# Kernel tuning notes

Hardware: AMD Instinct MI355X
Metric: run time of the kernel (lower is better)

## Reference

```python
import jax, jax.numpy as jnp
import numpy as np

N_HIGH = 4096
N_LOW = 262144
E_HIGH = 65536
E_LOW = 524288
IN_DIM = 128
OUT_DIM = 128
HEADS = 4
HEAD_DIM = OUT_DIM // HEADS
EPS = 1e-5
SCALE = np.float32(1.0 / np.sqrt(HEAD_DIM))


def _layernorm(x, w, b):
    m = jnp.mean(x, axis=-1, keepdims=True)
    v = jnp.var(x, axis=-1, keepdims=True)
    return (x - m) * jax.lax.rsqrt(v + EPS) * w + b


def _transformer_conv(x, edge_index, Wq, bq, Wk, bk, Wv, bv, Wskip, bskip, num_nodes):
    # PyG TransformerConv: q from target node, k/v from source node, per-head
    # softmax over incoming edges, concat heads, plus skip connection.
    q = (x @ Wq + bq).reshape(num_nodes, HEADS, HEAD_DIM)
    k = (x @ Wk + bk).reshape(num_nodes, HEADS, HEAD_DIM)
    v = (x @ Wv + bv).reshape(num_nodes, HEADS, HEAD_DIM)
    src, dst = edge_index[0], edge_index[1]
    score = jnp.einsum('ehd,ehd->eh', q[dst], k[src]) * SCALE  # [E, H]
    m = jax.ops.segment_max(score, dst, num_segments=num_nodes)
    e = jnp.exp(score - m[dst])
    denom = jax.ops.segment_sum(e, dst, num_segments=num_nodes)
    alpha = e / denom[dst]
    agg = jax.ops.segment_sum(alpha[:, :, None] * v[src], dst, num_segments=num_nodes)
    return agg.reshape(num_nodes, OUT_DIM) + x @ Wskip + bskip


def setup_inputs() -> dict:
    key = jax.random.key(0)
    ks = jax.random.split(key, 12)
    sw = np.float32(1.0 / np.sqrt(IN_DIM))
    sa = np.float32(1.0 / np.sqrt(2 * OUT_DIM))
    return {
        'high_emb': jax.random.normal(ks[0], (N_HIGH, IN_DIM), jnp.float32),
        'low_emb': jax.random.normal(ks[1], (N_LOW, IN_DIM), jnp.float32),
        'Wq': jax.random.normal(ks[2], (IN_DIM, OUT_DIM), jnp.float32) * sw,
        'bq': jnp.zeros((OUT_DIM,), jnp.float32),
        'Wk': jax.random.normal(ks[3], (IN_DIM, OUT_DIM), jnp.float32) * sw,
        'bk': jnp.zeros((OUT_DIM,), jnp.float32),
        'Wv': jax.random.normal(ks[4], (IN_DIM, OUT_DIM), jnp.float32) * sw,
        'bv': jnp.zeros((OUT_DIM,), jnp.float32),
        'Wskip': jax.random.normal(ks[5], (IN_DIM, OUT_DIM), jnp.float32) * sw,
        'bskip': jnp.zeros((OUT_DIM,), jnp.float32),
        'ln_w': jnp.ones((OUT_DIM,), jnp.float32),
        'ln_b': jnp.zeros((OUT_DIM,), jnp.float32),
        'w_lh': jax.random.normal(ks[6], (2 * OUT_DIM, 1), jnp.float32) * sa,
        'w_hl': jax.random.normal(ks[7], (2 * OUT_DIM, 1), jnp.float32) * sa,
        'edge_index_high': jax.random.randint(ks[8], (2, E_HIGH), 0, N_HIGH, jnp.int32),
        'edge_index_low': jax.random.randint(ks[9], (2, E_LOW), 0, N_LOW, jnp.int32),
        'batch': jnp.sort(jax.random.randint(ks[10], (N_LOW,), 0, N_HIGH, jnp.int32)),
    }


def reference(high_emb, low_emb, Wq, bq, Wk, bk, Wv, bv, Wskip, bskip, ln_w, ln_b, w_lh, w_hl, edge_index_high, edge_index_low, batch):
    h = _transformer_conv(high_emb, edge_index_high, Wq, bq, Wk, bk, Wv, bv, Wskip, bskip, N_HIGH)
    l = _transformer_conv(low_emb, edge_index_low, Wq, bq, Wk, bk, Wv, bv, Wskip, bskip, N_LOW)
    h = jax.nn.relu(_layernorm(h, ln_w, ln_b))
    l = jax.nn.relu(_layernorm(l, ln_w, ln_b))
    # global_mean_pool over low nodes per graph
    counts = jax.ops.segment_sum(jnp.ones((N_LOW,), jnp.float32), batch, num_segments=N_HIGH)
    pooled = jax.ops.segment_sum(l, batch, num_segments=N_HIGH) / jnp.maximum(counts, 1.0)[:, None]
    sim = jax.nn.sigmoid(jnp.concatenate([h, pooled], axis=1) @ w_lh)  # [N_HIGH, 1]
    high_out = sim * h + (1.0 - sim) * pooled
    # vectorized form of the per-graph loop: broadcast high node to its low nodes
    hb = h[batch]  # [N_LOW, OUT_DIM]
    a = jax.nn.sigmoid(jnp.concatenate([hb, l], axis=1) @ w_hl)  # [N_LOW, 1]
    low_out = a * l + (1.0 - a) * hb
    return (high_out, low_out)
```

## Files before the change

kernel.cpp:

```cpp
#include <hip/hip_runtime.h>
#include <hip/hip_bf16.h>
#include <math.h>

#define N_HIGH 4096
#define N_LOW 262144
#define E_HIGH 65536
#define E_LOW 524288
#define LN_EPS 1e-5f
#define ATT_SCALE 0.17677669529663687f

typedef short bf16x8 __attribute__((ext_vector_type(8)));
typedef float f32x4 __attribute__((ext_vector_type(4)));

__device__ __forceinline__ float bf2f(unsigned int u) {
    union { unsigned int i; float f; } v; v.i = u << 16; return v.f;
}
__device__ __forceinline__ unsigned short f2bf(float f) {
    union { unsigned int i; float f; } v; v.f = f;
    unsigned int r = (v.i + 0x7fffu + ((v.i >> 16) & 1u)) >> 16;
    return (unsigned short)r;
}
__device__ __forceinline__ float ldf(const void* p, size_t i, int isbf) {
    if (isbf) return bf2f(((const unsigned short*)p)[i]);
    return ((const float*)p)[i];
}
__device__ __forceinline__ float4 load4f(const void* p, size_t i, int isbf) {
    if (isbf) {
        uint2 u = *(const uint2*)((const unsigned short*)p + i);
        float4 r;
        r.x = bf2f(u.x & 0xffffu); r.y = bf2f(u.x >> 16);
        r.z = bf2f(u.y & 0xffffu); r.w = bf2f(u.y >> 16);
        return r;
    }
    return *(const float4*)((const float*)p + i);
}
__device__ __forceinline__ void stf(void* p, size_t i, float v, int isbf) {
    if (isbf) ((unsigned short*)p)[i] = f2bf(v);
    else      ((float*)p)[i] = v;
}

__global__ __launch_bounds__(256) void probe_dtype_kernel(
    const unsigned int* __restrict__ x, int* __restrict__ flag)
{
    __shared__ int cnt;
    if (threadIdx.x == 0) cnt = 0;
    __syncthreads();
    unsigned int b = (x[threadIdx.x] >> 8) & 0x7fu;
    if (b >= 60u && b <= 65u) atomicAdd(&cnt, 1);
    __syncthreads();
    if (threadIdx.x == 0) *flag = (cnt >= 128) ? 1 : 0;
}

__global__ __launch_bounds__(256) void prep_wt_kernel(
    const void* __restrict__ Wq, const void* __restrict__ Wk,
    const void* __restrict__ Wv, const void* __restrict__ Ws,
    unsigned short* __restrict__ Wt, const int* __restrict__ dflag)
{
    const int isbf = *dflag;
    const int g = blockIdx.x >> 3;
    const int slice = blockIdx.x & 7;
    const void* W = (g == 0) ? Wq : (g == 1) ? Wk : (g == 2) ? Wv : Ws;
    #pragma unroll
    for (int i = 0; i < 8; ++i) {
        int linear = i * 256 + threadIdx.x;
        int k = slice * 16 + (linear >> 7);
        int n = linear & 127;
        float v = ldf(W, (size_t)k * 128 + n, isbf);
        Wt[((size_t)g * 128 + n) * 128 + k] = f2bf(v);
    }
}

__global__ __launch_bounds__(256) void gemm_mfma_kernel(
    const void* __restrict__ x, const unsigned short* __restrict__ Wt,
    const void* __restrict__ bq, const void* __restrict__ bk,
    const void* __restrict__ bv, const void* __restrict__ bs,
    unsigned short* __restrict__ qkv, float* __restrict__ accv,
    const int* __restrict__ dflag)
{
    __shared__ unsigned short As[64 * 136];
    __shared__ unsigned short Bs[128 * 136];
    const int isbf = *dflag;
    const int tid = threadIdx.x;
    const int m0 = blockIdx.x * 64;

    #pragma unroll
    for (int i = 0; i < 8; ++i) {
        int linear = i * 256 + tid;
        int row = linear >> 5;
        int c4 = (linear & 31) << 2;
        float4 v = load4f(x, (size_t)(m0 + row) * 128 + c4, isbf);
        ushort4 s;
        s.x = f2bf(v.x); s.y = f2bf(v.y); s.z = f2bf(v.z); s.w = f2bf(v.w);
        *(ushort4*)&As[row * 136 + c4] = s;
    }

    const void* blist[4] = { bq, bk, bv, bs };

    const int lane = tid & 63;
    const int w = tid >> 6;
    const int wm = (w & 1) * 32;
    const int wn = (w >> 1) * 64;
    const int lr = lane & 15;
    const int lk = (lane >> 4) * 8;
    const int rbase = (lane >> 4) * 4;

    for (int c = 0; c < 4; ++c) {
        __syncthreads();
        #pragma unroll
        for (int i = 0; i < 8; ++i) {
            int linear = i * 256 + tid;
            int n = linear >> 4;
            int c8 = (linear & 15) << 3;
            uint4 v = *(const uint4*)&Wt[((size_t)c * 128 + n) * 128 + c8];
            *(uint4*)&Bs[n * 136 + c8] = v;
        }
        __syncthreads();

        f32x4 acc[2][4];
        #pragma unroll
        for (int a = 0; a < 2; ++a)
            #pragma unroll
            for (int b = 0; b < 4; ++b) acc[a][b] = (f32x4){0.f, 0.f, 0.f, 0.f};

        #pragma unroll
        for (int kk = 0; kk < 4; ++kk) {
            int k0 = kk * 32 + lk;
            bf16x8 af[2], bfv[4];
            #pragma unroll
            for (int im = 0; im < 2; ++im)
                af[im] = *(const bf16x8*)&As[(wm + im * 16 + lr) * 136 + k0];
            #pragma unroll
            for (int in = 0; in < 4; ++in)
                bfv[in] = *(const bf16x8*)&Bs[(wn + in * 16 + lr) * 136 + k0];
            #pragma unroll
            for (int im = 0; im < 2; ++im)
                #pragma unroll
                for (int in = 0; in < 4; ++in)
                    acc[im][in] = __builtin_amdgcn_mfma_f32_16x16x32_bf16(
                        af[im], bfv[in], acc[im][in], 0, 0, 0);
        }

        float bias[4];
        #pragma unroll
        for (int in = 0; in < 4; ++in) bias[in] = ldf(blist[c], wn + in * 16 + lr, isbf);

        #pragma unroll
        for (int im = 0; im < 2; ++im) {
            #pragma unroll
            for (int r = 0; r < 4; ++r) {
                int m = wm + im * 16 + rbase + r;
                size_t row = (size_t)(m0 + m);
                #pragma unroll
                for (int in = 0; in < 4; ++in) {
                    int n = wn + in * 16 + lr;
                    float val = acc[im][in][r] + bias[in];
                    if (c < 3) qkv[row * 384 + c * 128 + n] = f2bf(val);
                    else       accv[row * 128 + n] = val;
                }
            }
        }
    }
}

__global__ __launch_bounds__(256) void count_deg_kernel(
    const int* __restrict__ ei, int E, int* __restrict__ deg)
{
    int e = blockIdx.x * 256 + threadIdx.x;
    if (e >= E) return;
    atomicAdd(&deg[ei[E + e]], 1);
}

__global__ __launch_bounds__(256) void scan1_kernel(
    const int* __restrict__ deg, int* __restrict__ pre, int* __restrict__ bsum)
{
    __shared__ int wsum[4];
    int tid = threadIdx.x;
    int lane = tid & 63, w = tid >> 6;
    int base = blockIdx.x * 1024 + tid * 4;
    int4 v = *(const int4*)(deg + base);
    int s = v.x + v.y + v.z + v.w;
    int inc = s;
    #pragma unroll
    for (int m = 1; m < 64; m <<= 1) {
        int t = __shfl_up(inc, m, 64);
        if (lane >= m) inc += t;
    }
    if (lane == 63) wsum[w] = inc;
    __syncthreads();
    int woff = 0;
    #pragma unroll
    for (int j = 0; j < 4; ++j) if (j < w) woff += wsum[j];
    int excl = woff + inc - s;
    pre[base]     = excl;
    pre[base + 1] = excl + v.x;
    pre[base + 2] = excl + v.x + v.y;
    pre[base + 3] = excl + v.x + v.y + v.z;
    if (tid == 0) bsum[blockIdx.x] = wsum[0] + wsum[1] + wsum[2] + wsum[3];
}

__global__ void scan2_kernel(int* __restrict__ bsum, int NB)
{
    if (threadIdx.x == 0 && blockIdx.x == 0) {
        int run = 0;
        for (int i = 0; i < NB; ++i) { int t = bsum[i]; bsum[i] = run; run += t; }
    }
}

__global__ __launch_bounds__(256) void scan3_kernel(
    const int* __restrict__ pre, const int* __restrict__ bsum,
    int* __restrict__ off, int N)
{
    int i = blockIdx.x * 256 + threadIdx.x;
    if (i >= N) return;
    off[i] = pre[i] + bsum[i >> 10];
}

__global__ __launch_bounds__(256) void fill_csr_kernel(
    const int* __restrict__ ei, int E, int* __restrict__ off,
    int* __restrict__ csr)
{
    int e = blockIdx.x * 256 + threadIdx.x;
    if (e >= E) return;
    int dst = ei[E + e];
    int pos = atomicAdd(&off[dst], 1);
    csr[pos] = ei[e];
}

__global__ __launch_bounds__(256) void attn_gather_ln_kernel(
    const unsigned short* __restrict__ qkv, const int* __restrict__ csr_src,
    const int* __restrict__ off_end, const int* __restrict__ deg,
    const float* skip, const void* __restrict__ lnw,
    const void* __restrict__ lnb, unsigned short* out, int N,
    const int* __restrict__ dflag)
{
    const int isbf = *dflag;
    int lane = threadIdx.x & 63;
    int n = blockIdx.x * 4 + (threadIdx.x >> 6);
    if (n >= N) return;
    int end = off_end[n];
    int cnt = deg[n];
    int p = end - cnt;

    ushort2 qv = *(const ushort2*)(qkv + (long)n * 384 + 2 * lane);
    float q0 = bf2f(qv.x), q1 = bf2f(qv.y);
    float den = 0.f, a0 = 0.f, a1 = 0.f;

    for (; p + 1 < end; p += 2) {
        int s0 = csr_src[p], s1 = csr_src[p + 1];
        const unsigned short* b0 = qkv + (long)s0 * 384 + 2 * lane;
        const unsigned short* b1 = qkv + (long)s1 * 384 + 2 * lane;
        ushort2 k0 = *(const ushort2*)(b0 + 128);
        ushort2 k1 = *(const ushort2*)(b1 + 128);
        ushort2 v0 = *(const ushort2*)(b0 + 256);
        ushort2 v1 = *(const ushort2*)(b1 + 256);
        float p0 = q0 * bf2f(k0.x) + q1 * bf2f(k0.y);
        float p1 = q0 * bf2f(k1.x) + q1 * bf2f(k1.y);
        #pragma unroll
        for (int m = 1; m < 16; m <<= 1) {
            p0 += __shfl_xor(p0, m, 64);
            p1 += __shfl_xor(p1, m, 64);
        }
        float z0 = fminf(fmaxf(p0 * ATT_SCALE, -60.f), 60.f);
        float z1 = fminf(fmaxf(p1 * ATT_SCALE, -60.f), 60.f);
        float e0 = __expf(z0), e1 = __expf(z1);
        den += e0 + e1;
        a0 += e0 * bf2f(v0.x) + e1 * bf2f(v1.x);
        a1 += e0 * bf2f(v0.y) + e1 * bf2f(v1.y);
    }
    if (p < end) {
        int s0 = csr_src[p];
        const unsigned short* b0 = qkv + (long)s0 * 384 + 2 * lane;
        ushort2 k0 = *(const ushort2*)(b0 + 128);
        ushort2 v0 = *(const ushort2*)(b0 + 256);
        float p0 = q0 * bf2f(k0.x) + q1 * bf2f(k0.y);
        #pragma unroll
        for (int m = 1; m < 16; m <<= 1) p0 += __shfl_xor(p0, m, 64);
        float z0 = fminf(fmaxf(p0 * ATT_SCALE, -60.f), 60.f);
        float e0 = __expf(z0);
        den += e0;
        a0 += e0 * bf2f(v0.x);
        a1 += e0 * bf2f(v0.y);
    }

    float inv = (cnt > 0) ? 1.f / den : 0.f;
    float2 sk = *(const float2*)(skip + (long)n * 128 + 2 * lane);
    float x0 = a0 * inv + sk.x;
    float x1 = a1 * inv + sk.y;

    float s = x0 + x1, qq = x0 * x0 + x1 * x1;
    #pragma unroll
    for (int m = 1; m < 64; m <<= 1) {
        s += __shfl_xor(s, m, 64);
        qq += __shfl_xor(qq, m, 64);
    }
    float mean = s * (1.f / 128.f);
    float var = fmaxf(qq * (1.f / 128.f) - mean * mean, 0.f);
    float rs = rsqrtf(var + LN_EPS);
    float w0 = ldf(lnw, 2 * lane, isbf), w1 = ldf(lnw, 2 * lane + 1, isbf);
    float bb0 = ldf(lnb, 2 * lane, isbf), bb1 = ldf(lnb, 2 * lane + 1, isbf);
    float y0 = fmaxf((x0 - mean) * rs * w0 + bb0, 0.f);
    float y1 = fmaxf((x1 - mean) * rs * w1 + bb1, 0.f);
    unsigned short* o = out + (long)n * 256 + 2 * lane;
    o[0] = f2bf(y0);
    o[1] = f2bf(y1);
}

__global__ __launch_bounds__(128) void pool_kernel(
    const unsigned short* __restrict__ l, const int* __restrict__ batch,
    float* __restrict__ pooled)
{
    __shared__ int se[2];
    int g = blockIdx.x;
    if (threadIdx.x == 0) {
        int lo = 0, hi = N_LOW;
        while (lo < hi) { int mid = (lo + hi) >> 1; if (batch[mid] < g) lo = mid + 1; else hi = mid; }
        se[0] = lo;
        hi = N_LOW;
        while (lo < hi) { int mid = (lo + hi) >> 1; if (batch[mid] < g + 1) lo = mid + 1; else hi = mid; }
        se[1] = lo;
    }
    __syncthreads();
    int start = se[0], end = se[1];
    int d = threadIdx.x;
    float ssum = 0.f;
    for (int r = start; r < end; ++r) ssum += bf2f(l[(long)r * 256 + d]);
    int cnt = end - start;
    pooled[(long)g * 128 + d] = ssum / (float)(cnt > 0 ? cnt : 1);
}

__global__ __launch_bounds__(256) void high_out_kernel(
    const unsigned short* __restrict__ h, const float* __restrict__ pooled,
    const void* __restrict__ wlh, void* __restrict__ out,
    const int* __restrict__ dflag)
{
    const int isbf = *dflag;
    int lane = threadIdx.x & 63;
    int n = blockIdx.x * 4 + (threadIdx.x >> 6);
    if (n >= N_HIGH) return;
    float h0 = bf2f(h[(long)n * 256 + 2 * lane]);
    float h1 = bf2f(h[(long)n * 256 + 2 * lane + 1]);
    float2 pv = *(const float2*)(pooled + (long)n * 128 + 2 * lane);
    float s = h0 * ldf(wlh, 2 * lane, isbf) + h1 * ldf(wlh, 2 * lane + 1, isbf)
            + pv.x * ldf(wlh, 128 + 2 * lane, isbf) + pv.y * ldf(wlh, 128 + 2 * lane + 1, isbf);
    #pragma unroll
    for (int m = 1; m < 64; m <<= 1) s += __shfl_xor(s, m, 64);
    float sim = 1.f / (1.f + __expf(-s));
    stf(out, (size_t)n * 128 + 2 * lane,     sim * h0 + (1.f - sim) * pv.x, isbf);
    stf(out, (size_t)n * 128 + 2 * lane + 1, sim * h1 + (1.f - sim) * pv.y, isbf);
}

__global__ __launch_bounds__(256) void low_out_kernel(
    const unsigned short* __restrict__ l, const unsigned short* __restrict__ h,
    const int* __restrict__ batch, const void* __restrict__ whl,
    void* __restrict__ out, const int* __restrict__ dflag)
{
    const int isbf = *dflag;
    int lane = threadIdx.x & 63;
    int n = blockIdx.x * 4 + (threadIdx.x >> 6);
    if (n >= N_LOW) return;
    int g = batch[n];
    float l0 = bf2f(l[(long)n * 256 + 2 * lane]);
    float l1 = bf2f(l[(long)n * 256 + 2 * lane + 1]);
    float h0 = bf2f(h[(long)g * 256 + 2 * lane]);
    float h1 = bf2f(h[(long)g * 256 + 2 * lane + 1]);
    float s = h0 * ldf(whl, 2 * lane, isbf) + h1 * ldf(whl, 2 * lane + 1, isbf)
            + l0 * ldf(whl, 128 + 2 * lane, isbf) + l1 * ldf(whl, 128 + 2 * lane + 1, isbf);
    #pragma unroll
    for (int m = 1; m < 64; m <<= 1) s += __shfl_xor(s, m, 64);
    float a = 1.f / (1.f + __expf(-s));
    size_t base = (size_t)N_HIGH * 128 + (size_t)n * 128 + 2 * lane;
    stf(out, base,     a * l0 + (1.f - a) * h0, isbf);
    stf(out, base + 1, a * l1 + (1.f - a) * h1, isbf);
}

extern "C" void kernel_launch(void* const* d_in, const int* in_sizes, int n_in,
                              void* d_out, int out_size, void* d_ws, size_t ws_size,
                              hipStream_t stream)
{
    const void* high_emb = d_in[0];
    const void* low_emb  = d_in[1];
    const void* Wq = d_in[2];  const void* bq = d_in[3];
    const void* Wk = d_in[4];  const void* bk = d_in[5];
    const void* Wv = d_in[6];  const void* bv = d_in[7];
    const void* Ws = d_in[8];  const void* bs = d_in[9];
    const void* ln_w = d_in[10];
    const void* ln_b = d_in[11];
    const void* w_lh = d_in[12];
    const void* w_hl = d_in[13];
    const int* ei_high = (const int*)d_in[14];
    const int* ei_low  = (const int*)d_in[15];
    const int* batch   = (const int*)d_in[16];

    char* ws = (char*)d_ws;
    const size_t OFF_QKV_LOW  = 0;
    const size_t OFF_ACC_LOW  = 201326592;
    const size_t OFF_AUX      = 335544320;
    const size_t OFF_QKV_HIGH = 348127232;
    const size_t OFF_ACC_HIGH = 351272960;
    const size_t OFF_POOLED   = 354484224;
    const size_t OFF_FLAG     = 356581376;
    const size_t WS_NEEDED    = 356581632;
    if (ws_size < WS_NEEDED) return;

    unsigned short* qkv_low  = (unsigned short*)(ws + OFF_QKV_LOW);
    float*          acc_low  = (float*)(ws + OFF_ACC_LOW);
    unsigned short* qkv_high = (unsigned short*)(ws + OFF_QKV_HIGH);
    float*          acc_high = (float*)(ws + OFF_ACC_HIGH);
    float*          pooled   = (float*)(ws + OFF_POOLED);
    int*            dflag    = (int*)(ws + OFF_FLAG);

    unsigned short* Wt       = (unsigned short*)(ws + OFF_AUX);
    int* deg_low  = (int*)(ws + OFF_AUX +  262144);
    int* pre_low  = (int*)(ws + OFF_AUX + 1310720);
    int* off_low  = (int*)(ws + OFF_AUX + 2359296);
    int* csr_low  = (int*)(ws + OFF_AUX + 3407872);
    int* deg_high = (int*)(ws + OFF_AUX + 5505024);
    int* pre_high = (int*)(ws + OFF_AUX + 5521408);
    int* off_high = (int*)(ws + OFF_AUX + 5537792);
    int* csr_high = (int*)(ws + OFF_AUX + 5554176);
    int* bsum     = (int*)(ws + OFF_AUX + 5816320);

    unsigned short* l_low  = (unsigned short*)acc_low;
    unsigned short* h_high = (unsigned short*)acc_high;

    hipMemsetAsync(deg_low, 0, (size_t)N_LOW * sizeof(int), stream);
    hipMemsetAsync(deg_high, 0, (size_t)N_HIGH * sizeof(int), stream);

    probe_dtype_kernel<<<1, 256, 0, stream>>>((const unsigned int*)high_emb, dflag);

    count_deg_kernel<<<E_LOW / 256, 256, 0, stream>>>(ei_low, E_LOW, deg_low);
    count_deg_kernel<<<E_HIGH / 256, 256, 0, stream>>>(ei_high, E_HIGH, deg_high);

    scan1_kernel<<<N_LOW / 1024, 256, 0, stream>>>(deg_low, pre_low, bsum);
    scan2_kernel<<<1, 64, 0, stream>>>(bsum, N_LOW / 1024);
    scan3_kernel<<<N_LOW / 256, 256, 0, stream>>>(pre_low, bsum, off_low, N_LOW);

    scan1_kernel<<<N_HIGH / 1024, 256, 0, stream>>>(deg_high, pre_high, bsum);
    scan2_kernel<<<1, 64, 0, stream>>>(bsum, N_HIGH / 1024);
    scan3_kernel<<<N_HIGH / 256, 256, 0, stream>>>(pre_high, bsum, off_high, N_HIGH);

    fill_csr_kernel<<<E_LOW / 256, 256, 0, stream>>>(ei_low, E_LOW, off_low, csr_low);
    fill_csr_kernel<<<E_HIGH / 256, 256, 0, stream>>>(ei_high, E_HIGH, off_high, csr_high);

    prep_wt_kernel<<<32, 256, 0, stream>>>(Wq, Wk, Wv, Ws, Wt, dflag);

    gemm_mfma_kernel<<<N_HIGH / 64, 256, 0, stream>>>(
        high_emb, Wt, bq, bk, bv, bs, qkv_high, acc_high, dflag);
    gemm_mfma_kernel<<<N_LOW / 64, 256, 0, stream>>>(
        low_emb, Wt, bq, bk, bv, bs, qkv_low, acc_low, dflag);

    attn_gather_ln_kernel<<<N_HIGH / 4, 256, 0, stream>>>(
        qkv_high, csr_high, off_high, deg_high, acc_high, ln_w, ln_b,
        h_high, N_HIGH, dflag);
    attn_gather_ln_kernel<<<N_LOW / 4, 256, 0, stream>>>(
        qkv_low, csr_low, off_low, deg_low, acc_low, ln_w, ln_b,
        l_low, N_LOW, dflag);

    pool_kernel<<<N_HIGH, 128, 0, stream>>>(l_low, batch, pooled);

    high_out_kernel<<<N_HIGH / 4, 256, 0, stream>>>(h_high, pooled, w_lh, d_out, dflag);
    low_out_kernel<<<N_LOW / 4, 256, 0, stream>>>(l_low, h_high, batch, w_hl, d_out, dflag);
}
```

Baseline: 763.3 us.

## Store skip in bf16, use 16 lanes per node with 16-byte vector gathers

The skip-connection output of the GEMM is now written as bf16 instead of fp32, and the layer-norm result overwrites it in place with a 128-element row stride. The attention-gather, layernorm and low-output kernels move from one 64-lane wave per node to 16 lanes per node, each lane loading 8 bf16 values with uint4 loads. LayerNorm weights and w_hl are pre-converted to fp32 once by an extra block in prep_wt. The aim is fewer gather transactions, fewer shuffle reduction steps and less skip/output traffic. The cost is extra bf16 rounding of the skip term.

```diff
diff --git a/kernel.cpp b/kernel.cpp
--- a/kernel.cpp
+++ b/kernel.cpp
@@ -38,6 +38,20 @@
     if (isbf) ((unsigned short*)p)[i] = f2bf(v);
     else      ((float*)p)[i] = v;
 }
+__device__ __forceinline__ void unpack8(uint4 u, float* f) {
+    f[0] = bf2f(u.x & 0xffffu); f[1] = bf2f(u.x >> 16);
+    f[2] = bf2f(u.y & 0xffffu); f[3] = bf2f(u.y >> 16);
+    f[4] = bf2f(u.z & 0xffffu); f[5] = bf2f(u.z >> 16);
+    f[6] = bf2f(u.w & 0xffffu); f[7] = bf2f(u.w >> 16);
+}
+__device__ __forceinline__ uint4 pack8(const float* f) {
+    uint4 u;
+    u.x = (unsigned)f2bf(f[0]) | ((unsigned)f2bf(f[1]) << 16);
+    u.y = (unsigned)f2bf(f[2]) | ((unsigned)f2bf(f[3]) << 16);
+    u.z = (unsigned)f2bf(f[4]) | ((unsigned)f2bf(f[5]) << 16);
+    u.w = (unsigned)f2bf(f[6]) | ((unsigned)f2bf(f[7]) << 16);
+    return u;
+}
 
 __global__ __launch_bounds__(256) void probe_dtype_kernel(
     const unsigned int* __restrict__ x, int* __restrict__ flag)
@@ -54,9 +68,18 @@
 __global__ __launch_bounds__(256) void prep_wt_kernel(
     const void* __restrict__ Wq, const void* __restrict__ Wk,
     const void* __restrict__ Wv, const void* __restrict__ Ws,
-    unsigned short* __restrict__ Wt, const int* __restrict__ dflag)
+    const void* __restrict__ lnw, const void* __restrict__ lnb,
+    const void* __restrict__ whl,
+    unsigned short* __restrict__ Wt, float* __restrict__ lnwbf,
+    float* __restrict__ whlf, const int* __restrict__ dflag)
 {
     const int isbf = *dflag;
+    if (blockIdx.x >= 32) {
+        int t = threadIdx.x;
+        lnwbf[t] = (t < 128) ? ldf(lnw, t, isbf) : ldf(lnb, t - 128, isbf);
+        whlf[t] = ldf(whl, t, isbf);
+        return;
+    }
     const int g = blockIdx.x >> 3;
     const int slice = blockIdx.x & 7;
     const void* W = (g == 0) ? Wq : (g == 1) ? Wk : (g == 2) ? Wv : Ws;
@@ -74,7 +97,7 @@
     const void* __restrict__ x, const unsigned short* __restrict__ Wt,
     const void* __restrict__ bq, const void* __restrict__ bk,
     const void* __restrict__ bv, const void* __restrict__ bs,
-    unsigned short* __restrict__ qkv, float* __restrict__ accv,
+    unsigned short* __restrict__ qkv, unsigned short* __restrict__ accv,
     const int* __restrict__ dflag)
 {
     __shared__ unsigned short As[64 * 136];
@@ -155,7 +178,7 @@
                     int n = wn + in * 16 + lr;
                     float val = acc[im][in][r] + bias[in];
                     if (c < 3) qkv[row * 384 + c * 128 + n] = f2bf(val);
-                    else       accv[row * 128 + n] = val;
+                    else       accv[row * 128 + n] = f2bf(val);
                 }
             }
         }
@@ -229,80 +252,91 @@
 __global__ __launch_bounds__(256) void attn_gather_ln_kernel(
     const unsigned short* __restrict__ qkv, const int* __restrict__ csr_src,
     const int* __restrict__ off_end, const int* __restrict__ deg,
-    const float* skip, const void* __restrict__ lnw,
-    const void* __restrict__ lnb, unsigned short* out, int N,
-    const int* __restrict__ dflag)
-{
-    const int isbf = *dflag;
-    int lane = threadIdx.x & 63;
-    int n = blockIdx.x * 4 + (threadIdx.x >> 6);
+    unsigned short* skip_out, const float* __restrict__ lnwbf, int N)
+{
+    int il = threadIdx.x & 15;
+    int n = blockIdx.x * 16 + (threadIdx.x >> 4);
     if (n >= N) return;
     int end = off_end[n];
     int cnt = deg[n];
     int p = end - cnt;
 
-    ushort2 qv = *(const ushort2*)(qkv + (long)n * 384 + 2 * lane);
-    float q0 = bf2f(qv.x), q1 = bf2f(qv.y);
-    float den = 0.f, a0 = 0.f, a1 = 0.f;
-
-    for (; p + 1 < end; p += 2) {
-        int s0 = csr_src[p], s1 = csr_src[p + 1];
-        const unsigned short* b0 = qkv + (long)s0 * 384 + 2 * lane;
-        const unsigned short* b1 = qkv + (long)s1 * 384 + 2 * lane;
-        ushort2 k0 = *(const ushort2*)(b0 + 128);
-        ushort2 k1 = *(const ushort2*)(b1 + 128);
-        ushort2 v0 = *(const ushort2*)(b0 + 256);
-        ushort2 v1 = *(const ushort2*)(b1 + 256);
-        float p0 = q0 * bf2f(k0.x) + q1 * bf2f(k0.y);
-        float p1 = q0 * bf2f(k1.x) + q1 * bf2f(k1.y);
-        #pragma unroll
-        for (int m = 1; m < 16; m <<= 1) {
-            p0 += __shfl_xor(p0, m, 64);
-            p1 += __shfl_xor(p1, m, 64);
-        }
-        float z0 = fminf(fmaxf(p0 * ATT_SCALE, -60.f), 60.f);
-        float z1 = fminf(fmaxf(p1 * ATT_SCALE, -60.f), 60.f);
-        float e0 = __expf(z0), e1 = __expf(z1);
+    float qf[8];
+    unpack8(*(const uint4*)(qkv + (long)n * 384 + 8 * il), qf);
+    float acc[8] = {0.f, 0.f, 0.f, 0.f, 0.f, 0.f, 0.f, 0.f};
+    float den = 0.f;
+
+    int it = 0;
+    for (; it + 1 < cnt; it += 2) {
+        int s0 = csr_src[p + it];
+        int s1 = csr_src[p + it + 1];
+        const unsigned short* b0 = qkv + (long)s0 * 384 + 8 * il;
+        const unsigned short* b1 = qkv + (long)s1 * 384 + 8 * il;
+        uint4 k0w = *(const uint4*)(b0 + 128);
+        uint4 v0w = *(const uint4*)(b0 + 256);
+        uint4 k1w = *(const uint4*)(b1 + 128);
+        uint4 v1w = *(const uint4*)(b1 + 256);
+        float kf[8], vf[8], kg[8], vg[8];
+        unpack8(k0w, kf); unpack8(v0w, vf);
+        unpack8(k1w, kg); unpack8(v1w, vg);
+        float p0 = 0.f, p1 = 0.f;
+        #pragma unroll
+        for (int j = 0; j < 8; ++j) { p0 += qf[j] * kf[j]; p1 += qf[j] * kg[j]; }
+        p0 += __shfl_xor(p0, 1, 64); p1 += __shfl_xor(p1, 1, 64);
+        p0 += __shfl_xor(p0, 2, 64); p1 += __shfl_xor(p1, 2, 64);
+        float e0 = __expf(fminf(fmaxf(p0 * ATT_SCALE, -60.f), 60.f));
+        float e1 = __expf(fminf(fmaxf(p1 * ATT_SCALE, -60.f), 60.f));
         den += e0 + e1;
-        a0 += e0 * bf2f(v0.x) + e1 * bf2f(v1.x);
-        a1 += e0 * bf2f(v0.y) + e1 * bf2f(v1.y);
-    }
-    if (p < end) {
-        int s0 = csr_src[p];
-        const unsigned short* b0 = qkv + (long)s0 * 384 + 2 * lane;
-        ushort2 k0 = *(const ushort2*)(b0 + 128);
-        ushort2 v0 = *(const ushort2*)(b0 + 256);
-        float p0 = q0 * bf2f(k0.x) + q1 * bf2f(k0.y);
-        #pragma unroll
-        for (int m = 1; m < 16; m <<= 1) p0 += __shfl_xor(p0, m, 64);
-        float z0 = fminf(fmaxf(p0 * ATT_SCALE, -60.f), 60.f);
-        float e0 = __expf(z0);
+        #pragma unroll
+        for (int j = 0; j < 8; ++j) acc[j] += e0 * vf[j] + e1 * vg[j];
+    }
+    if (it < cnt) {
+        int s0 = csr_src[p + it];
+        const unsigned short* b0 = qkv + (long)s0 * 384 + 8 * il;
+        uint4 k0w = *(const uint4*)(b0 + 128);
+        uint4 v0w = *(const uint4*)(b0 + 256);
+        float kf[8], vf[8];
+        unpack8(k0w, kf); unpack8(v0w, vf);
+        float p0 = 0.f;
+        #pragma unroll
+        for (int j = 0; j < 8; ++j) p0 += qf[j] * kf[j];
+        p0 += __shfl_xor(p0, 1, 64);
+        p0 += __shfl_xor(p0, 2, 64);
+        float e0 = __expf(fminf(fmaxf(p0 * ATT_SCALE, -60.f), 60.f));
         den += e0;
-        a0 += e0 * bf2f(v0.x);
-        a1 += e0 * bf2f(v0.y);
+        #pragma unroll
+        for (int j = 0; j < 8; ++j) acc[j] += e0 * vf[j];
     }
 
     float inv = (cnt > 0) ? 1.f / den : 0.f;
-    float2 sk = *(const float2*)(skip + (long)n * 128 + 2 * lane);
-    float x0 = a0 * inv + sk.x;
-    float x1 = a1 * inv + sk.y;
-
-    float s = x0 + x1, qq = x0 * x0 + x1 * x1;
-    #pragma unroll
-    for (int m = 1; m < 64; m <<= 1) {
+    float x[8];
+    unpack8(*(const uint4*)(skip_out + (long)n * 128 + 8 * il), x);
+    float s = 0.f, qq = 0.f;
+    #pragma unroll
+    for (int j = 0; j < 8; ++j) {
+        x[j] = acc[j] * inv + x[j];
+        s += x[j];
+        qq += x[j] * x[j];
+    }
+    #pragma unroll
+    for (int m = 1; m < 16; m <<= 1) {
         s += __shfl_xor(s, m, 64);
         qq += __shfl_xor(qq, m, 64);
     }
     float mean = s * (1.f / 128.f);
     float var = fmaxf(qq * (1.f / 128.f) - mean * mean, 0.f);
     float rs = rsqrtf(var + LN_EPS);
-    float w0 = ldf(lnw, 2 * lane, isbf), w1 = ldf(lnw, 2 * lane + 1, isbf);
-    float bb0 = ldf(lnb, 2 * lane, isbf), bb1 = ldf(lnb, 2 * lane + 1, isbf);
-    float y0 = fmaxf((x0 - mean) * rs * w0 + bb0, 0.f);
-    float y1 = fmaxf((x1 - mean) * rs * w1 + bb1, 0.f);
-    unsigned short* o = out + (long)n * 256 + 2 * lane;
-    o[0] = f2bf(y0);
-    o[1] = f2bf(y1);
+    float4 wA = *(const float4*)(lnwbf + 8 * il);
+    float4 wB = *(const float4*)(lnwbf + 8 * il + 4);
+    float4 bA = *(const float4*)(lnwbf + 128 + 8 * il);
+    float4 bB = *(const float4*)(lnwbf + 128 + 8 * il + 4);
+    float wv[8] = {wA.x, wA.y, wA.z, wA.w, wB.x, wB.y, wB.z, wB.w};
+    float bv[8] = {bA.x, bA.y, bA.z, bA.w, bB.x, bB.y, bB.z, bB.w};
+    float y[8];
+    #pragma unroll
+    for (int j = 0; j < 8; ++j)
+        y[j] = fmaxf((x[j] - mean) * rs * wv[j] + bv[j], 0.f);
+    *(uint4*)(skip_out + (long)n * 128 + 8 * il) = pack8(y);
 }
 
 __global__ __launch_bounds__(128) void pool_kernel(
@@ -322,10 +356,17 @@
     __syncthreads();
     int start = se[0], end = se[1];
     int d = threadIdx.x;
-    float ssum = 0.f;
-    for (int r = start; r < end; ++r) ssum += bf2f(l[(long)r * 256 + d]);
+    float s0 = 0.f, s1 = 0.f, s2 = 0.f, s3 = 0.f;
+    int r = start;
+    for (; r + 3 < end; r += 4) {
+        s0 += bf2f(l[(long)r * 128 + d]);
+        s1 += bf2f(l[(long)(r + 1) * 128 + d]);
+        s2 += bf2f(l[(long)(r + 2) * 128 + d]);
+        s3 += bf2f(l[(long)(r + 3) * 128 + d]);
+    }
+    for (; r < end; ++r) s0 += bf2f(l[(long)r * 128 + d]);
     int cnt = end - start;
-    pooled[(long)g * 128 + d] = ssum / (float)(cnt > 0 ? cnt : 1);
+    pooled[(long)g * 128 + d] = ((s0 + s1) + (s2 + s3)) / (float)(cnt > 0 ? cnt : 1);
 }
 
 __global__ __launch_bounds__(256) void high_out_kernel(
@@ -337,8 +378,8 @@
     int lane = threadIdx.x & 63;
     int n = blockIdx.x * 4 + (threadIdx.x >> 6);
     if (n >= N_HIGH) return;
-    float h0 = bf2f(h[(long)n * 256 + 2 * lane]);
-    float h1 = bf2f(h[(long)n * 256 + 2 * lane + 1]);
+    float h0 = bf2f(h[(long)n * 128 + 2 * lane]);
+    float h1 = bf2f(h[(long)n * 128 + 2 * lane + 1]);
     float2 pv = *(const float2*)(pooled + (long)n * 128 + 2 * lane);
     float s = h0 * ldf(wlh, 2 * lane, isbf) + h1 * ldf(wlh, 2 * lane + 1, isbf)
             + pv.x * ldf(wlh, 128 + 2 * lane, isbf) + pv.y * ldf(wlh, 128 + 2 * lane + 1, isbf);
@@ -351,26 +392,39 @@
 
 __global__ __launch_bounds__(256) void low_out_kernel(
     const unsigned short* __restrict__ l, const unsigned short* __restrict__ h,
-    const int* __restrict__ batch, const void* __restrict__ whl,
+    const int* __restrict__ batch, const float* __restrict__ whlf,
     void* __restrict__ out, const int* __restrict__ dflag)
 {
     const int isbf = *dflag;
-    int lane = threadIdx.x & 63;
-    int n = blockIdx.x * 4 + (threadIdx.x >> 6);
+    int il = threadIdx.x & 15;
+    int n = blockIdx.x * 16 + (threadIdx.x >> 4);
     if (n >= N_LOW) return;
     int g = batch[n];
-    float l0 = bf2f(l[(long)n * 256 + 2 * lane]);
-    float l1 = bf2f(l[(long)n * 256 + 2 * lane + 1]);
-    float h0 = bf2f(h[(long)g * 256 + 2 * lane]);
-    float h1 = bf2f(h[(long)g * 256 + 2 * lane + 1]);
-    float s = h0 * ldf(whl, 2 * lane, isbf) + h1 * ldf(whl, 2 * lane + 1, isbf)
-            + l0 * ldf(whl, 128 + 2 * lane, isbf) + l1 * ldf(whl, 128 + 2 * lane + 1, isbf);
-    #pragma unroll
-    for (int m = 1; m < 64; m <<= 1) s += __shfl_xor(s, m, 64);
+    float lf[8], hf[8];
+    unpack8(*(const uint4*)(l + (long)n * 128 + 8 * il), lf);
+    unpack8(*(const uint4*)(h + (long)g * 128 + 8 * il), hf);
+    float4 wh0 = *(const float4*)(whlf + 8 * il);
+    float4 wh1 = *(const float4*)(whlf + 8 * il + 4);
+    float4 wl0 = *(const float4*)(whlf + 128 + 8 * il);
+    float4 wl1 = *(const float4*)(whlf + 128 + 8 * il + 4);
+    float s = hf[0] * wh0.x + hf[1] * wh0.y + hf[2] * wh0.z + hf[3] * wh0.w
+            + hf[4] * wh1.x + hf[5] * wh1.y + hf[6] * wh1.z + hf[7] * wh1.w
+            + lf[0] * wl0.x + lf[1] * wl0.y + lf[2] * wl0.z + lf[3] * wl0.w
+            + lf[4] * wl1.x + lf[5] * wl1.y + lf[6] * wl1.z + lf[7] * wl1.w;
+    #pragma unroll
+    for (int m = 1; m < 16; m <<= 1) s += __shfl_xor(s, m, 64);
     float a = 1.f / (1.f + __expf(-s));
-    size_t base = (size_t)N_HIGH * 128 + (size_t)n * 128 + 2 * lane;
-    stf(out, base,     a * l0 + (1.f - a) * h0, isbf);
-    stf(out, base + 1, a * l1 + (1.f - a) * h1, isbf);
+    float y[8];
+    #pragma unroll
+    for (int j = 0; j < 8; ++j) y[j] = a * lf[j] + (1.f - a) * hf[j];
+    size_t base = (size_t)N_HIGH * 128 + (size_t)n * 128 + 8 * il;
+    if (isbf) {
+        *(uint4*)((unsigned short*)out + base) = pack8(y);
+    } else {
+        float* o = (float*)out + base;
+        *(float4*)o       = (float4){y[0], y[1], y[2], y[3]};
+        *(float4*)(o + 4) = (float4){y[4], y[5], y[6], y[7]};
+    }
 }
 
 extern "C" void kernel_launch(void* const* d_in, const int* in_sizes, int n_in,
@@ -403,13 +457,15 @@
     if (ws_size < WS_NEEDED) return;
 
     unsigned short* qkv_low  = (unsigned short*)(ws + OFF_QKV_LOW);
-    float*          acc_low  = (float*)(ws + OFF_ACC_LOW);
+    unsigned short* acc_low  = (unsigned short*)(ws + OFF_ACC_LOW);
     unsigned short* qkv_high = (unsigned short*)(ws + OFF_QKV_HIGH);
-    float*          acc_high = (float*)(ws + OFF_ACC_HIGH);
+    unsigned short* acc_high = (unsigned short*)(ws + OFF_ACC_HIGH);
     float*          pooled   = (float*)(ws + OFF_POOLED);
     int*            dflag    = (int*)(ws + OFF_FLAG);
 
-    unsigned short* Wt       = (unsigned short*)(ws + OFF_AUX);
+    unsigned short* Wt    = (unsigned short*)(ws + OFF_AUX);
+    float* lnwbf = (float*)(ws + OFF_AUX + 131072);
+    float* whlf  = (float*)(ws + OFF_AUX + 132096);
     int* deg_low  = (int*)(ws + OFF_AUX +  262144);
     int* pre_low  = (int*)(ws + OFF_AUX + 1310720);
     int* off_low  = (int*)(ws + OFF_AUX + 2359296);
@@ -420,8 +476,8 @@
     int* csr_high = (int*)(ws + OFF_AUX + 5554176);
     int* bsum     = (int*)(ws + OFF_AUX + 5816320);
 
-    unsigned short* l_low  = (unsigned short*)acc_low;
-    unsigned short* h_high = (unsigned short*)acc_high;
+    unsigned short* l_low  = acc_low;
+    unsigned short* h_high = acc_high;
 
     hipMemsetAsync(deg_low, 0, (size_t)N_LOW * sizeof(int), stream);
     hipMemsetAsync(deg_high, 0, (size_t)N_HIGH * sizeof(int), stream);
@@ -442,22 +498,21 @@
     fill_csr_kernel<<<E_LOW / 256, 256, 0, stream>>>(ei_low, E_LOW, off_low, csr_low);
     fill_csr_kernel<<<E_HIGH / 256, 256, 0, stream>>>(ei_high, E_HIGH, off_high, csr_high);
 
-    prep_wt_kernel<<<32, 256, 0, stream>>>(Wq, Wk, Wv, Ws, Wt, dflag);
+    prep_wt_kernel<<<33, 256, 0, stream>>>(Wq, Wk, Wv, Ws, ln_w, ln_b, w_hl,
+                                           Wt, lnwbf, whlf, dflag);
 
     gemm_mfma_kernel<<<N_HIGH / 64, 256, 0, stream>>>(
         high_emb, Wt, bq, bk, bv, bs, qkv_high, acc_high, dflag);
     gemm_mfma_kernel<<<N_LOW / 64, 256, 0, stream>>>(
         low_emb, Wt, bq, bk, bv, bs, qkv_low, acc_low, dflag);
 
-    attn_gather_ln_kernel<<<N_HIGH / 4, 256, 0, stream>>>(
-        qkv_high, csr_high, off_high, deg_high, acc_high, ln_w, ln_b,
-        h_high, N_HIGH, dflag);
-    attn_gather_ln_kernel<<<N_LOW / 4, 256, 0, stream>>>(
-        qkv_low, csr_low, off_low, deg_low, acc_low, ln_w, ln_b,
-        l_low, N_LOW, dflag);
+    attn_gather_ln_kernel<<<N_HIGH / 16, 256, 0, stream>>>(
+        qkv_high, csr_high, off_high, deg_high, acc_high, lnwbf, N_HIGH);
+    attn_gather_ln_kernel<<<N_LOW / 16, 256, 0, stream>>>(
+        qkv_low, csr_low, off_low, deg_low, acc_low, lnwbf, N_LOW);
 
     pool_kernel<<<N_HIGH, 128, 0, stream>>>(l_low, batch, pooled);
 
     high_out_kernel<<<N_HIGH / 4, 256, 0, stream>>>(h_high, pooled, w_lh, d_out, dflag);
-    low_out_kernel<<<N_LOW / 4, 256, 0, stream>>>(l_low, h_high, batch, w_hl, d_out, dflag);
-}
+    low_out_kernel<<<N_LOW / 16, 256, 0, stream>>>(l_low, h_high, batch, whlf, d_out, dflag);
+}
```

Result: faster. 615.2 us (-19.4%).
